# Kernel optimization log

Measured on AMD Instinct MI355X. Metric: run time of the kernel, lower is better.

Reference implementation:

```python
import jax, jax.numpy as jnp
import numpy as np

D_MODEL = 1024
NUM_HEADS = 16
D_K = D_MODEL // NUM_HEADS


def setup_inputs() -> dict:
    key = jax.random.key(0)
    ks = jax.random.split(key, 9)
    s = 1.0 / np.sqrt(D_MODEL)
    x = jax.random.normal(ks[0], (1, 4096, D_MODEL), dtype=jnp.float32)
    Wq = jax.random.uniform(ks[1], (D_MODEL, D_MODEL), jnp.float32, -s, s)
    bq = jax.random.uniform(ks[2], (D_MODEL,), jnp.float32, -s, s)
    Wk = jax.random.uniform(ks[3], (D_MODEL, D_MODEL), jnp.float32, -s, s)
    bk = jax.random.uniform(ks[4], (D_MODEL,), jnp.float32, -s, s)
    Wv = jax.random.uniform(ks[5], (D_MODEL, D_MODEL), jnp.float32, -s, s)
    bv = jax.random.uniform(ks[6], (D_MODEL,), jnp.float32, -s, s)
    Wo = jax.random.uniform(ks[7], (D_MODEL, D_MODEL), jnp.float32, -s, s)
    bo = jax.random.uniform(ks[8], (D_MODEL,), jnp.float32, -s, s)
    return {"x": x, "Wq": Wq, "bq": bq, "Wk": Wk, "bk": bk,
            "Wv": Wv, "bv": bv, "Wo": Wo, "bo": bo}


def reference(x, Wq, bq, Wk, bk, Wv, bv, Wo, bo):
    B, S, _ = x.shape
    scale = jnp.sqrt(jnp.asarray(D_K, dtype=x.dtype))
    # projections (torch Linear: y = x @ W.T + b)
    q = (x @ Wq.T + bq).reshape(B, S, NUM_HEADS, D_K).transpose(0, 2, 1, 3)
    k = (x @ Wk.T + bk).reshape(B, S, NUM_HEADS, D_K).transpose(0, 2, 1, 3)
    v = (x @ Wv.T + bv).reshape(B, S, NUM_HEADS, D_K).transpose(0, 2, 1, 3)
    # [B, H, S, S] naive scores, causal mask, softmax
    scores = jnp.einsum('bhqd,bhkd->bhqk', q, k) / scale
    causal = jnp.tril(jnp.ones((S, S), dtype=bool))
    scores = jnp.where(causal, scores, jnp.asarray(-jnp.inf, dtype=scores.dtype))
    probs = jax.nn.softmax(scores, axis=-1)
    out = jnp.einsum('bhqk,bhkd->bhqd', probs, v)
    out = out.transpose(0, 2, 1, 3).reshape(B, S, D_MODEL)
    return out @ Wo.T + bo
```

## Files before the change

### kernel.cpp

```cpp
#include <hip/hip_runtime.h>
#include <math.h>

#define SEQ 4096
#define DMODEL 1024
#define NH 16
#define DK 64
#define LDP 72

typedef __bf16    bf16x8 __attribute__((ext_vector_type(8)));
typedef float     f32x4  __attribute__((ext_vector_type(4)));
typedef _Float16  h16x4  __attribute__((ext_vector_type(4)));
typedef _Float16  h16x8  __attribute__((ext_vector_type(8)));

#define GLOAD_LDS16(g, l) __builtin_amdgcn_global_load_lds(                     \
    (const __attribute__((address_space(1))) unsigned int*)(g),                 \
    (__attribute__((address_space(3))) unsigned int*)(l), 16, 0, 0)

__global__ __launch_bounds__(256)
void cvt_all(const float* __restrict__ x, const float* __restrict__ Wq,
             const float* __restrict__ Wk, const float* __restrict__ Wv,
             const float* __restrict__ Wo, __bf16* __restrict__ dst)
{
    const size_t M1 = 1u << 20;
    const size_t e = ((size_t)blockIdx.x * 256 + threadIdx.x) * 8;
    const float* src; size_t off;
    if      (e < 4*M1) { src = x;  off = e;        }
    else if (e < 5*M1) { src = Wq; off = e - 4*M1; }
    else if (e < 6*M1) { src = Wk; off = e - 5*M1; }
    else if (e < 7*M1) { src = Wv; off = e - 6*M1; }
    else               { src = Wo; off = e - 7*M1; }
    const float4 f0 = *reinterpret_cast<const float4*>(&src[off]);
    const float4 f1 = *reinterpret_cast<const float4*>(&src[off + 4]);
    bf16x8 pk;
    pk[0]=(__bf16)f0.x; pk[1]=(__bf16)f0.y; pk[2]=(__bf16)f0.z; pk[3]=(__bf16)f0.w;
    pk[4]=(__bf16)f1.x; pk[5]=(__bf16)f1.y; pk[6]=(__bf16)f1.z; pk[7]=(__bf16)f1.w;
    *reinterpret_cast<bf16x8*>(&dst[e]) = pk;
}

__device__ __forceinline__ void gemm_core128(const __bf16* __restrict__ A,
                                             const __bf16* __restrict__ W,
                                             int m0, int n0, int t,
                                             __bf16* AsF, __bf16* BsF,
                                             f32x4 acc[4][4])
{
    const int w = t >> 6, lane = t & 63, l15 = lane & 15, quad = lane >> 4;
    const int wm = (w & 1) * 64, wn = (w >> 1) * 64;
    const int lr = lane >> 3, lc = lane & 7;
    for (int k0 = 0; k0 < DMODEL; k0 += 64) {
        __syncthreads();
        #pragma unroll
        for (int p = 0; p < 4; ++p) {
            const int n = w*4 + p;
            const int r = n*8 + lr;
            const int cl = lc ^ (r & 7);
            GLOAD_LDS16(&A[(size_t)(m0 + r) * DMODEL + k0 + cl*8], &AsF[n*512]);
            GLOAD_LDS16(&W[(size_t)(n0 + r) * DMODEL + k0 + cl*8], &BsF[n*512]);
        }
        __syncthreads();
        #pragma unroll
        for (int kb = 0; kb < 2; ++kb) {
            const int phys = ((kb*4 + quad) ^ (l15 & 7)) * 8;
            bf16x8 af[4], bfr[4];
            #pragma unroll
            for (int i = 0; i < 4; ++i) {
                af[i]  = *reinterpret_cast<const bf16x8*>(&AsF[(wm + i*16 + l15)*64 + phys]);
                bfr[i] = *reinterpret_cast<const bf16x8*>(&BsF[(wn + i*16 + l15)*64 + phys]);
            }
            #pragma unroll
            for (int ms = 0; ms < 4; ++ms)
                #pragma unroll
                for (int ns = 0; ns < 4; ++ns)
                    acc[ms][ns] = __builtin_amdgcn_mfma_f32_16x16x32_bf16(af[ms], bfr[ns], acc[ms][ns], 0, 0, 0);
        }
    }
}

__global__ __launch_bounds__(256, 3)
void gemm_qkv(const __bf16* __restrict__ xb, const __bf16* __restrict__ Wcat,
              const float* __restrict__ bq, const float* __restrict__ bk,
              const float* __restrict__ bv,
              _Float16* __restrict__ Qh, _Float16* __restrict__ Kh, _Float16* __restrict__ Vth)
{
    __shared__ __bf16 SM[4*64*LDP];
    __bf16* AsF = SM;
    __bf16* BsF = SM + 8192;
    const int t = threadIdx.x;
    const int n0g = blockIdx.x * 128;
    const int m0  = blockIdx.y * 128;
    const int which = n0g >> 10;
    const int n_in  = n0g & 1023;

    f32x4 acc[4][4] = {};
    gemm_core128(xb, Wcat, m0, n0g, t, AsF, BsF, acc);

    const int w = t >> 6, lane = t & 63, l15 = lane & 15, quad = lane >> 4;
    const int wm = (w & 1) * 64, wn = (w >> 1) * 64;
    const float* bias = (which == 0) ? bq : (which == 1) ? bk : bv;
    float br[4];
    #pragma unroll
    for (int ns = 0; ns < 4; ++ns) br[ns] = bias[n_in + wn + ns*16 + l15];

    if (which == 2) {
        #pragma unroll
        for (int ms = 0; ms < 4; ++ms)
            #pragma unroll
            for (int ns = 0; ns < 4; ++ns) {
                h16x4 pk;
                #pragma unroll
                for (int rg = 0; rg < 4; ++rg) pk[rg] = (_Float16)(acc[ms][ns][rg] + br[ns]);
                *reinterpret_cast<h16x4*>(
                    &Vth[(size_t)(n_in + wn + ns*16 + l15) * SEQ + m0 + wm + ms*16 + quad*4]) = pk;
            }
    } else {
        const float s = (which == 0) ? 0.1803368787f : 1.0f;
        _Float16* C = (which == 0) ? Qh : Kh;
        __syncthreads();
        _Float16* tile = (_Float16*)SM + w * 64 * LDP;
        #pragma unroll
        for (int ms = 0; ms < 4; ++ms)
            #pragma unroll
            for (int ns = 0; ns < 4; ++ns)
                #pragma unroll
                for (int rg = 0; rg < 4; ++rg)
                    tile[(ms*16 + quad*4 + rg) * LDP + ns*16 + l15] =
                        (_Float16)((acc[ms][ns][rg] + br[ns]) * s);
        asm volatile("s_waitcnt lgkmcnt(0)" ::: "memory");
        const int er = lane >> 3, ec = (lane & 7) * 8;
        #pragma unroll
        for (int p = 0; p < 8; ++p) {
            const h16x8 v = *reinterpret_cast<const h16x8*>(&tile[(er + p*8) * LDP + ec]);
            *reinterpret_cast<h16x8*>(
                &C[(size_t)(m0 + wm + er + p*8) * DMODEL + n_in + wn + ec]) = v;
        }
    }
}

__device__ __forceinline__ void gemm_core64(const __bf16* __restrict__ A,
                                            const __bf16* __restrict__ W,
                                            int m0, int n0, int t,
                                            __bf16* AsF, __bf16* BsF,
                                            f32x4 acc[2][4])
{
    const int w = t >> 6, lane = t & 63, l15 = lane & 15, quad = lane >> 4;
    const int lr = lane >> 3, lc = lane & 7;
    for (int k0 = 0; k0 < DMODEL; k0 += 64) {
        __syncthreads();
        #pragma unroll
        for (int p = 0; p < 4; ++p) {
            const int n = w*4 + p;
            const int r = n*8 + lr;
            const int cl = lc ^ (r & 7);
            GLOAD_LDS16(&A[(size_t)(m0 + r) * DMODEL + k0 + cl*8], &AsF[n*512]);
        }
        #pragma unroll
        for (int p = 0; p < 2; ++p) {
            const int n = w*2 + p;
            const int r = n*8 + lr;
            const int cl = lc ^ (r & 7);
            GLOAD_LDS16(&W[(size_t)(n0 + r) * DMODEL + k0 + cl*8], &BsF[n*512]);
        }
        __syncthreads();
        #pragma unroll
        for (int kb = 0; kb < 2; ++kb) {
            const int phys = ((kb*4 + quad) ^ (l15 & 7)) * 8;
            bf16x8 af0 = *reinterpret_cast<const bf16x8*>(&AsF[(w*32 + l15)*64 + phys]);
            bf16x8 af1 = *reinterpret_cast<const bf16x8*>(&AsF[(w*32 + 16 + l15)*64 + phys]);
            #pragma unroll
            for (int ns = 0; ns < 4; ++ns) {
                const bf16x8 bfr = *reinterpret_cast<const bf16x8*>(&BsF[(ns*16 + l15)*64 + phys]);
                acc[0][ns] = __builtin_amdgcn_mfma_f32_16x16x32_bf16(af0, bfr, acc[0][ns], 0, 0, 0);
                acc[1][ns] = __builtin_amdgcn_mfma_f32_16x16x32_bf16(af1, bfr, acc[1][ns], 0, 0, 0);
            }
        }
    }
}

__global__ __launch_bounds__(256, 4)
void gemm_out(const __bf16* __restrict__ Ob, const __bf16* __restrict__ Wob,
              const float* __restrict__ bo, float* __restrict__ out)
{
    __shared__ __bf16 AsF[128*64];
    __shared__ __bf16 BsF[64*64];
    const int t = threadIdx.x;
    const int n0 = blockIdx.x * 64;
    const int m0 = blockIdx.y * 128;

    f32x4 acc[2][4] = {};
    gemm_core64(Ob, Wob, m0, n0, t, AsF, BsF, acc);

    const int lane = t & 63, l15 = lane & 15, quad = lane >> 4, w = t >> 6;
    float br[4];
    #pragma unroll
    for (int ns = 0; ns < 4; ++ns) br[ns] = bo[n0 + ns*16 + l15];
    #pragma unroll
    for (int ms = 0; ms < 2; ++ms)
        #pragma unroll
        for (int ns = 0; ns < 4; ++ns)
            #pragma unroll
            for (int rg = 0; rg < 4; ++rg)
                out[(size_t)(m0 + w*32 + ms*16 + quad*4 + rg) * DMODEL + n0 + ns*16 + l15] =
                    acc[ms][ns][rg] + br[ns];
}

__global__ __launch_bounds__(256, 3)
void attn_mfma(const _Float16* __restrict__ Q, const _Float16* __restrict__ K,
               const _Float16* __restrict__ Vt, __bf16* __restrict__ O,
               float* __restrict__ part, float* __restrict__ lpart)
{
    __shared__ _Float16 KsF[64*64];
    __shared__ _Float16 Vts[64][LDP];

    const int t = threadIdx.x;
    const int w = t >> 6;
    const int lane = t & 63, l15 = lane & 15, quad = lane >> 4;
    const int lr = lane >> 3, lc = lane & 7;
    const int h = blockIdx.y;
    const int u = blockIdx.x;
    int qt, g;
    if      (u < 16) { qt = 16 + u; g = 0; }
    else if (u < 32) { qt = u;      g = 1; }
    else             { qt = 47 - u; g = 0; }
    const int tstart = g * 32;
    const int tlast  = 2*qt + 1;
    const int tend   = (tlast < tstart + 31) ? tlast : (tstart + 31);
    const int s0 = qt*128 + w*16;
    const int s1 = s0 + 64;

    h16x8 bq8[2][2];
    #pragma unroll
    for (int kb = 0; kb < 2; ++kb) {
        bq8[0][kb] = *reinterpret_cast<const h16x8*>(
            &Q[(size_t)(s0 + l15) * DMODEL + h*DK + kb*32 + quad*8]);
        bq8[1][kb] = *reinterpret_cast<const h16x8*>(
            &Q[(size_t)(s1 + l15) * DMODEL + h*DK + kb*32 + quad*8]);
    }

    f32x4 acc[2][4] = {};
    float lsum[2] = {0.f, 0.f};

    for (int tk = tstart; tk <= tend; ++tk) {
        const int j0 = tk * 64;
        __syncthreads();
        #pragma unroll
        for (int p = 0; p < 2; ++p) {
            const int idx = t + p * 256;
            const int r = idx >> 3, c = (idx & 7) * 8;
            *reinterpret_cast<h16x8*>(&Vts[r][c]) =
                *reinterpret_cast<const h16x8*>(&Vt[(size_t)(h*DK + r) * SEQ + j0 + c]);
        }
        #pragma unroll
        for (int p = 0; p < 2; ++p) {
            const int n = w*2 + p;
            const int r = n*8 + lr;
            const int cl = lc ^ (r & 7);
            GLOAD_LDS16(&K[(size_t)(j0 + r) * DMODEL + h*DK + cl*8], &KsF[n*512]);
        }
        __syncthreads();

        const bool act0 = (j0 <= s0 + 15);
        const bool msk0 = (j0 + 63 > s0);
        const bool msk1 = (j0 + 63 > s1);
        const int rel0 = s0 - j0 + l15;
        const int rel1 = s1 - j0 + l15;

        h16x4 ap[2][4];
        #pragma unroll
        for (int st = 0; st < 4; ++st) {
            const h16x8 ak0 = *reinterpret_cast<const h16x8*>(
                &KsF[(st*16 + l15)*64 + ((quad ^ (l15 & 7)))*8]);
            const h16x8 ak1 = *reinterpret_cast<const h16x8*>(
                &KsF[(st*16 + l15)*64 + (((4 + quad) ^ (l15 & 7)))*8]);
            {
                f32x4 cc = {0.f, 0.f, 0.f, 0.f};
                cc = __builtin_amdgcn_mfma_f32_16x16x32_f16(ak0, bq8[1][0], cc, 0, 0, 0);
                cc = __builtin_amdgcn_mfma_f32_16x16x32_f16(ak1, bq8[1][1], cc, 0, 0, 0);
                #pragma unroll
                for (int rg = 0; rg < 4; ++rg) {
                    float pv = exp2f(cc[rg]);
                    if (msk1 && (st*16 + quad*4 + rg > rel1)) pv = 0.f;
                    lsum[1] += pv;
                    ap[1][st][rg] = (_Float16)pv;
                }
            }
            if (act0) {
                f32x4 cc = {0.f, 0.f, 0.f, 0.f};
                cc = __builtin_amdgcn_mfma_f32_16x16x32_f16(ak0, bq8[0][0], cc, 0, 0, 0);
                cc = __builtin_amdgcn_mfma_f32_16x16x32_f16(ak1, bq8[0][1], cc, 0, 0, 0);
                #pragma unroll
                for (int rg = 0; rg < 4; ++rg) {
                    float pv = exp2f(cc[rg]);
                    if (msk0 && (st*16 + quad*4 + rg > rel0)) pv = 0.f;
                    lsum[0] += pv;
                    ap[0][st][rg] = (_Float16)pv;
                }
            }
        }

        #pragma unroll
        for (int ds_ = 0; ds_ < 4; ++ds_) {
            #pragma unroll
            for (int st = 0; st < 4; ++st) {
                const h16x4 bv = *reinterpret_cast<const h16x4*>(
                    &Vts[ds_*16 + l15][st*16 + quad*4]);
                acc[1][ds_] = __builtin_amdgcn_mfma_f32_16x16x16f16(ap[1][st], bv, acc[1][ds_], 0, 0, 0);
                if (act0)
                    acc[0][ds_] = __builtin_amdgcn_mfma_f32_16x16x16f16(ap[0][st], bv, acc[0][ds_], 0, 0, 0);
            }
        }
    }

    float ls[2];
    #pragma unroll
    for (int s = 0; s < 2; ++s) {
        float v = lsum[s];
        v += __shfl_xor(v, 16);
        v += __shfl_xor(v, 32);
        ls[s] = v;
    }

    if (qt < 16) {
        #pragma unroll
        for (int s = 0; s < 2; ++s) {
            const int base = s ? s1 : s0;
            #pragma unroll
            for (int rg = 0; rg < 4; ++rg) {
                const float dn = __shfl(ls[s], quad*4 + rg);
                const float inv = 1.0f / dn;
                const size_t row = (size_t)(base + quad*4 + rg) * DMODEL + h * DK;
                #pragma unroll
                for (int ds_ = 0; ds_ < 4; ++ds_)
                    O[row + ds_*16 + l15] = (__bf16)(acc[s][ds_][rg] * inv);
            }
        }
    } else {
        const int unit = (h*16 + (qt - 16))*2 + g;
        const size_t pb = (size_t)unit * 8192;
        #pragma unroll
        for (int s = 0; s < 2; ++s) {
            #pragma unroll
            for (int rg = 0; rg < 4; ++rg) {
                const int lrow = s*64 + w*16 + quad*4 + rg;
                #pragma unroll
                for (int ds_ = 0; ds_ < 4; ++ds_)
                    part[pb + lrow*64 + ds_*16 + l15] = acc[s][ds_][rg];
            }
            if (quad == 0) lpart[unit*128 + s*64 + w*16 + l15] = ls[s];
        }
    }
}

__global__ __launch_bounds__(256)
void attn_combine(const float* __restrict__ part, const float* __restrict__ lpart,
                  __bf16* __restrict__ O)
{
    const int t = threadIdx.x;
    const int qtp = blockIdx.x;
    const int h = blockIdx.y;
    const int u0 = (h*16 + qtp)*2;
    const size_t b0 = (size_t)u0 * 8192;
    const size_t b1 = b0 + 8192;
    const int r  = t >> 1;
    const int d0 = (t & 1) * 32;

    const float l = lpart[u0*128 + r] + lpart[(u0 + 1)*128 + r];
    const float inv = 1.0f / l;
    const size_t grow = (size_t)((16 + qtp)*128 + r) * DMODEL + h*64 + d0;
    #pragma unroll
    for (int i = 0; i < 4; ++i) {
        bf16x8 pk;
        #pragma unroll
        for (int j = 0; j < 2; ++j) {
            const float4 p0 = *reinterpret_cast<const float4*>(&part[b0 + r*64 + d0 + i*8 + j*4]);
            const float4 p1 = *reinterpret_cast<const float4*>(&part[b1 + r*64 + d0 + i*8 + j*4]);
            pk[j*4+0] = (__bf16)((p0.x + p1.x) * inv);
            pk[j*4+1] = (__bf16)((p0.y + p1.y) * inv);
            pk[j*4+2] = (__bf16)((p0.z + p1.z) * inv);
            pk[j*4+3] = (__bf16)((p0.w + p1.w) * inv);
        }
        *reinterpret_cast<bf16x8*>(&O[grow + i*8]) = pk;
    }
}

extern "C" void kernel_launch(void* const* d_in, const int* in_sizes, int n_in,
                              void* d_out, int out_size, void* d_ws, size_t ws_size,
                              hipStream_t stream) {
    const float* x  = (const float*)d_in[0];
    const float* Wq = (const float*)d_in[1];
    const float* bq = (const float*)d_in[2];
    const float* Wk = (const float*)d_in[3];
    const float* bk = (const float*)d_in[4];
    const float* Wv = (const float*)d_in[5];
    const float* bv = (const float*)d_in[6];
    const float* Wo = (const float*)d_in[7];
    const float* bo = (const float*)d_in[8];
    float* out = (float*)d_out;

    const size_t M1 = 1u << 20;
    __bf16* base = (__bf16*)d_ws;
    __bf16*    xb   = base;
    __bf16*    Wcat = base + 4*M1;
    __bf16*    Wob  = base + 7*M1;
    _Float16*  Qh   = (_Float16*)(base + 8*M1);
    _Float16*  Kh   = (_Float16*)(base + 12*M1);
    _Float16*  Vth  = (_Float16*)(base + 16*M1);
    __bf16*    Ob   = base + 20*M1;
    float*     lpart = (float*)(base + 24*M1);
    float*     part  = out;

    cvt_all<<<4096, 256, 0, stream>>>(x, Wq, Wk, Wv, Wo, base);
    gemm_qkv<<<dim3(24, 32), 256, 0, stream>>>(xb, Wcat, bq, bk, bv, Qh, Kh, Vth);
    attn_mfma<<<dim3(48, NH), 256, 0, stream>>>(Qh, Kh, Vth, Ob, part, lpart);
    attn_combine<<<dim3(16, NH), 256, 0, stream>>>(part, lpart, Ob);
    gemm_out<<<dim3(16, 32), 256, 0, stream>>>(Ob, Wob, bo, out);
}
```

Measured before the change: 233.0 us.

## Double-buffer K/V tiles via async LDS loads and compute row sums with MFMA

Replaces the single-buffered K and V tiles with double-buffered LDS tiles filled by direct global-to-LDS loads. The next tile is prefetched while the current one is computed, cutting one of the two barriers per iteration. V now uses the same XOR-swizzled layout as K. The softmax denominator is accumulated by an extra MFMA against a ones vector instead of scalar adds and shuffles, and the fp16 conversion uses a packed round-toward-zero instruction. In exchange it doubles the LDS footprint, adds an MFMA per sub-tile, and sums the denominator from fp16-rounded values.

Measured after the change: 229.2 us. Within noise of the previous version (-1.6%).

```diff
diff --git a/kernel.cpp b/kernel.cpp
--- a/kernel.cpp
+++ b/kernel.cpp
@@ -9,12 +9,19 @@
 
 typedef __bf16    bf16x8 __attribute__((ext_vector_type(8)));
 typedef float     f32x4  __attribute__((ext_vector_type(4)));
+typedef __fp16    fp16x2 __attribute__((ext_vector_type(2)));
+typedef _Float16  h16x2  __attribute__((ext_vector_type(2)));
 typedef _Float16  h16x4  __attribute__((ext_vector_type(4)));
 typedef _Float16  h16x8  __attribute__((ext_vector_type(8)));
 
 #define GLOAD_LDS16(g, l) __builtin_amdgcn_global_load_lds(                     \
     (const __attribute__((address_space(1))) unsigned int*)(g),                 \
     (__attribute__((address_space(3))) unsigned int*)(l), 16, 0, 0)
+
+__device__ __forceinline__ h16x2 cvt_pk_h16(float a, float b) {
+    fp16x2 r = __builtin_amdgcn_cvt_pkrtz(a, b);
+    return __builtin_bit_cast(h16x2, r);
+}
 
 __global__ __launch_bounds__(256)
 void cvt_all(const float* __restrict__ x, const float* __restrict__ Wq,
@@ -207,8 +214,8 @@
                const _Float16* __restrict__ Vt, __bf16* __restrict__ O,
                float* __restrict__ part, float* __restrict__ lpart)
 {
-    __shared__ _Float16 KsF[64*64];
-    __shared__ _Float16 Vts[64][LDP];
+    __shared__ _Float16 KsF[2][64*64];
+    __shared__ _Float16 VsF[2][64*64];
 
     const int t = threadIdx.x;
     const int w = t >> 6;
@@ -235,28 +242,34 @@
             &Q[(size_t)(s1 + l15) * DMODEL + h*DK + kb*32 + quad*8]);
     }
 
+    const int cl = lc ^ lr;
+    const int rA = (w*2 + 0)*8 + lr, rB = (w*2 + 1)*8 + lr;
+    const int dA = (w*2 + 0)*512,   dB = (w*2 + 1)*512;
+    const _Float16* kpA = &K [(size_t)(tstart*64 + rA) * DMODEL + h*DK + cl*8];
+    const _Float16* kpB = &K [(size_t)(tstart*64 + rB) * DMODEL + h*DK + cl*8];
+    const _Float16* vpA = &Vt[(size_t)(h*DK + rA) * SEQ + tstart*64 + cl*8];
+    const _Float16* vpB = &Vt[(size_t)(h*DK + rB) * SEQ + tstart*64 + cl*8];
+
+#define STAGE_KV(bi) do {                                     \
+        GLOAD_LDS16(kpA, &KsF[bi][dA]);                       \
+        GLOAD_LDS16(kpB, &KsF[bi][dB]);                       \
+        GLOAD_LDS16(vpA, &VsF[bi][dA]);                       \
+        GLOAD_LDS16(vpB, &VsF[bi][dB]);                       \
+        kpA += (size_t)64*DMODEL; kpB += (size_t)64*DMODEL;   \
+        vpA += 64; vpB += 64; } while (0)
+
     f32x4 acc[2][4] = {};
-    float lsum[2] = {0.f, 0.f};
-
-    for (int tk = tstart; tk <= tend; ++tk) {
+    f32x4 accl[2] = {};
+    const h16x4 vone = {(_Float16)1.f, (_Float16)1.f, (_Float16)1.f, (_Float16)1.f};
+
+    STAGE_KV(0);
+    __syncthreads();
+
+    int pbuf = 0;
+    for (int tk = tstart; tk <= tend; ++tk, pbuf ^= 1) {
+        if (tk < tend) STAGE_KV(pbuf ^ 1);
+
         const int j0 = tk * 64;
-        __syncthreads();
-        #pragma unroll
-        for (int p = 0; p < 2; ++p) {
-            const int idx = t + p * 256;
-            const int r = idx >> 3, c = (idx & 7) * 8;
-            *reinterpret_cast<h16x8*>(&Vts[r][c]) =
-                *reinterpret_cast<const h16x8*>(&Vt[(size_t)(h*DK + r) * SEQ + j0 + c]);
-        }
-        #pragma unroll
-        for (int p = 0; p < 2; ++p) {
-            const int n = w*2 + p;
-            const int r = n*8 + lr;
-            const int cl = lc ^ (r & 7);
-            GLOAD_LDS16(&K[(size_t)(j0 + r) * DMODEL + h*DK + cl*8], &KsF[n*512]);
-        }
-        __syncthreads();
-
         const bool act0 = (j0 <= s0 + 15);
         const bool msk0 = (j0 + 63 > s0);
         const bool msk1 = (j0 + 63 > s1);
@@ -267,32 +280,40 @@
         #pragma unroll
         for (int st = 0; st < 4; ++st) {
             const h16x8 ak0 = *reinterpret_cast<const h16x8*>(
-                &KsF[(st*16 + l15)*64 + ((quad ^ (l15 & 7)))*8]);
+                &KsF[pbuf][(st*16 + l15)*64 + ((quad ^ (l15 & 7)))*8]);
             const h16x8 ak1 = *reinterpret_cast<const h16x8*>(
-                &KsF[(st*16 + l15)*64 + (((4 + quad) ^ (l15 & 7)))*8]);
+                &KsF[pbuf][(st*16 + l15)*64 + (((4 + quad) ^ (l15 & 7)))*8]);
             {
                 f32x4 cc = {0.f, 0.f, 0.f, 0.f};
                 cc = __builtin_amdgcn_mfma_f32_16x16x32_f16(ak0, bq8[1][0], cc, 0, 0, 0);
                 cc = __builtin_amdgcn_mfma_f32_16x16x32_f16(ak1, bq8[1][1], cc, 0, 0, 0);
+                float pv[4];
                 #pragma unroll
                 for (int rg = 0; rg < 4; ++rg) {
-                    float pv = exp2f(cc[rg]);
-                    if (msk1 && (st*16 + quad*4 + rg > rel1)) pv = 0.f;
-                    lsum[1] += pv;
-                    ap[1][st][rg] = (_Float16)pv;
+                    float e = exp2f(cc[rg]);
+                    if (msk1 && (st*16 + quad*4 + rg > rel1)) e = 0.f;
+                    pv[rg] = e;
                 }
+                const h16x2 lo = cvt_pk_h16(pv[0], pv[1]);
+                const h16x2 hi = cvt_pk_h16(pv[2], pv[3]);
+                ap[1][st] = (h16x4){lo[0], lo[1], hi[0], hi[1]};
+                accl[1] = __builtin_amdgcn_mfma_f32_16x16x16f16(ap[1][st], vone, accl[1], 0, 0, 0);
             }
             if (act0) {
                 f32x4 cc = {0.f, 0.f, 0.f, 0.f};
                 cc = __builtin_amdgcn_mfma_f32_16x16x32_f16(ak0, bq8[0][0], cc, 0, 0, 0);
                 cc = __builtin_amdgcn_mfma_f32_16x16x32_f16(ak1, bq8[0][1], cc, 0, 0, 0);
+                float pv[4];
                 #pragma unroll
                 for (int rg = 0; rg < 4; ++rg) {
-                    float pv = exp2f(cc[rg]);
-                    if (msk0 && (st*16 + quad*4 + rg > rel0)) pv = 0.f;
-                    lsum[0] += pv;
-                    ap[0][st][rg] = (_Float16)pv;
+                    float e = exp2f(cc[rg]);
+                    if (msk0 && (st*16 + quad*4 + rg > rel0)) e = 0.f;
+                    pv[rg] = e;
                 }
+                const h16x2 lo = cvt_pk_h16(pv[0], pv[1]);
+                const h16x2 hi = cvt_pk_h16(pv[2], pv[3]);
+                ap[0][st] = (h16x4){lo[0], lo[1], hi[0], hi[1]};
+                accl[0] = __builtin_amdgcn_mfma_f32_16x16x16f16(ap[0][st], vone, accl[0], 0, 0, 0);
             }
         }
 
@@ -301,22 +322,16 @@
             #pragma unroll
             for (int st = 0; st < 4; ++st) {
                 const h16x4 bv = *reinterpret_cast<const h16x4*>(
-                    &Vts[ds_*16 + l15][st*16 + quad*4]);
+                    &VsF[pbuf][(ds_*16 + l15)*64 +
+                               (((st*2 + (quad >> 1)) ^ (l15 & 7)))*8 + (quad & 1)*4]);
                 acc[1][ds_] = __builtin_amdgcn_mfma_f32_16x16x16f16(ap[1][st], bv, acc[1][ds_], 0, 0, 0);
                 if (act0)
                     acc[0][ds_] = __builtin_amdgcn_mfma_f32_16x16x16f16(ap[0][st], bv, acc[0][ds_], 0, 0, 0);
             }
         }
-    }
-
-    float ls[2];
-    #pragma unroll
-    for (int s = 0; s < 2; ++s) {
-        float v = lsum[s];
-        v += __shfl_xor(v, 16);
-        v += __shfl_xor(v, 32);
-        ls[s] = v;
-    }
+        __syncthreads();
+    }
+#undef STAGE_KV
 
     if (qt < 16) {
         #pragma unroll
@@ -324,8 +339,7 @@
             const int base = s ? s1 : s0;
             #pragma unroll
             for (int rg = 0; rg < 4; ++rg) {
-                const float dn = __shfl(ls[s], quad*4 + rg);
-                const float inv = 1.0f / dn;
+                const float inv = 1.0f / accl[s][rg];
                 const size_t row = (size_t)(base + quad*4 + rg) * DMODEL + h * DK;
                 #pragma unroll
                 for (int ds_ = 0; ds_ < 4; ++ds_)
@@ -334,7 +348,7 @@
         }
     } else {
         const int unit = (h*16 + (qt - 16))*2 + g;
-        const size_t pb = (size_t)unit * 8192;
+        const size_t pbase = (size_t)unit * 8192;
         #pragma unroll
         for (int s = 0; s < 2; ++s) {
             #pragma unroll
@@ -342,9 +356,13 @@
                 const int lrow = s*64 + w*16 + quad*4 + rg;
                 #pragma unroll
                 for (int ds_ = 0; ds_ < 4; ++ds_)
-                    part[pb + lrow*64 + ds_*16 + l15] = acc[s][ds_][rg];
-            }
-            if (quad == 0) lpart[unit*128 + s*64 + w*16 + l15] = ls[s];
+                    part[pbase + lrow*64 + ds_*16 + l15] = acc[s][ds_][rg];
+            }
+            if (l15 == 0) {
+                #pragma unroll
+                for (int rg = 0; rg < 4; ++rg)
+                    lpart[unit*128 + s*64 + w*16 + quad*4 + rg] = accl[s][rg];
+            }
         }
     }
 }
```
